# Kernel tuning notes

Measured on AMD Instinct MI355X. Metric: run time of the kernel, lower is better.

The kernel has to match this reference:

```python
import jax, jax.numpy as jnp
import numpy as np

NUM_EXPERTS = 8
EMBED_DIM = 512
NUM_LAYERS = 2
LN_EPS = 1e-5


def _all_pairs_hyperedges(E):
    # static 'all_pairs' strategy: one hyperedge per unordered expert pair
    nodes, edges = [], []
    eid = 0
    for i in range(E):
        for j in range(i + 1, E):
            nodes += [i, j]
            edges += [eid, eid]
            eid += 1
    return np.asarray(nodes, np.int32), np.asarray(edges, np.int32)


def setup_inputs() -> dict:
    key = jax.random.key(0)
    ks = jax.random.split(key, 4)
    B, L, E, D = 8, 1024, NUM_EXPERTS, EMBED_DIM
    nodes, edges = _all_pairs_hyperedges(E)
    return {
        "expert_outputs": jax.random.normal(ks[0], (B, L, E, D), jnp.float32),
        # HypergraphConv: lin has bias=False, conv bias is separate
        "hgnn_w": jax.random.normal(ks[1], (NUM_LAYERS, D, D), jnp.float32) * 0.02,
        "hgnn_b": jnp.zeros((NUM_LAYERS, D), jnp.float32),
        # combiner: Linear(D,D) -> GELU -> LayerNorm(D)
        "comb_w": jax.random.normal(ks[2], (D, D), jnp.float32) * 0.02,
        "comb_b": jnp.zeros((D,), jnp.float32),
        "ln_gamma": jnp.ones((D,), jnp.float32),
        "ln_beta": jnp.zeros((D,), jnp.float32),
        "nodes_idx": jnp.asarray(nodes),
        "edges_idx": jnp.asarray(edges),
    }


def _hypergraph_conv(h, W, b, nodes_idx, edges_idx, num_edges, d_inv, b_inv):
    # h: [N, E, D] with N = B*L token-graphs sharing the static hyperedge structure.
    # PyG HypergraphConv (no attention, unit edge weights):
    #   out = D^{-1} H B^{-1} H^T (h @ W^T) + b
    x = jnp.einsum('ned,fd->nef', h, W)  # lin(x), bias=False
    N, E, D = x.shape
    # node -> hyperedge scatter-add, scaled by inverse hyperedge degree B^{-1}
    m = jnp.zeros((N, num_edges, D), x.dtype)
    m = m.at[:, edges_idx].add(x[:, nodes_idx]) * b_inv[None, :, None]
    # hyperedge -> node scatter-add, scaled by inverse node degree D^{-1}
    out = jnp.zeros((N, E, D), x.dtype)
    out = out.at[:, nodes_idx].add(m[:, edges_idx]) * d_inv[None, :, None]
    return out + b


def reference(expert_outputs, hgnn_w, hgnn_b, comb_w, comb_b, ln_gamma, ln_beta, nodes_idx, edges_idx):
    B, L, E, D = expert_outputs.shape
    num_edges = nodes_idx.shape[0] // 2  # all_pairs: exactly 2 nodes per hyperedge
    # degree normalizations (unit hyperedge weights)
    deg = jnp.zeros((E,), expert_outputs.dtype).at[nodes_idx].add(1.0)
    d_inv = jnp.where(deg > 0, 1.0 / deg, 0.0)
    edeg = jnp.zeros((num_edges,), expert_outputs.dtype).at[edges_idx].add(1.0)
    b_inv = jnp.where(edeg > 0, 1.0 / edeg, 0.0)

    h = expert_outputs.reshape(B * L, E, D)
    for l in range(hgnn_w.shape[0]):
        h = _hypergraph_conv(h, hgnn_w[l], hgnn_b[l], nodes_idx, edges_idx, num_edges, d_inv, b_inv)

    pooled = h.reshape(B, L, E, D).mean(axis=2)  # [B, L, D]
    z = jax.nn.gelu(pooled @ comb_w.T + comb_b, approximate=False)  # torch nn.GELU = exact
    mu = jnp.mean(z, axis=-1, keepdims=True)
    var = jnp.var(z, axis=-1, keepdims=True)
    return (z - mu) / jnp.sqrt(var + LN_EPS) * ln_gamma + ln_beta
```

## Files before the change

kernel.cpp:

```cpp
#include <hip/hip_runtime.h>
#include <hip/hip_bf16.h>
#include <math.h>


#define DD 512
#define NTOK 8192

typedef short s16x8 __attribute__((ext_vector_type(8)));
typedef short s16x4 __attribute__((ext_vector_type(4)));
typedef float f32x4 __attribute__((ext_vector_type(4)));

static __device__ __forceinline__ short f2bf(float x) {
  unsigned u = __builtin_bit_cast(unsigned, x);
  unsigned r = (u + 0x7fffu + ((u >> 16) & 1u)) >> 16;
  return (short)r;
}

static __device__ __forceinline__ void do_cast4(const float* __restrict__ src,
                                                short* __restrict__ dst, int i) {
  int j = i << 2;
  f32x4 v = *(const f32x4*)(src + j);
  s16x4 o;
  o[0] = f2bf(v[0]); o[1] = f2bf(v[1]); o[2] = f2bf(v[2]); o[3] = f2bf(v[3]);
  *(s16x4*)(dst + j) = o;
}

static __device__ __forceinline__ void do_mv(const float* __restrict__ M,
                                             const float* __restrict__ v,
                                             const float* __restrict__ add,
                                             float* __restrict__ outv,
                                             int gtid) {
  int w = gtid >> 6, l = gtid & 63;
  if (w >= DD) return;
  float s = 0.f;
  for (int k = l; k < DD; k += 64) s += M[(size_t)w * DD + k] * v[k];
#pragma unroll
  for (int m = 32; m; m >>= 1) s += __shfl_xor(s, m);
  if (l == 0) outv[w] = s + add[w];
}

__global__ __launch_bounds__(256) void prep1_kernel(
    const float* __restrict__ w1, const float* __restrict__ w2,
    const float* __restrict__ wc, const float* __restrict__ b1,
    const float* __restrict__ b2, short* __restrict__ w1t,
    short* __restrict__ w2b, short* __restrict__ wcb,
    float* __restrict__ tmpv) {
  int b = blockIdx.x, tid = threadIdx.x;
  if (b < 256) {
    __shared__ float t[32][33];
    int bx = b & 15, by = b >> 4;
    int tx = tid & 31, ty8 = tid >> 5;
    int r0 = by * 32, c0 = bx * 32;
#pragma unroll
    for (int j = 0; j < 4; ++j) {
      int r = ty8 * 4 + j;
      t[r][tx] = w1[(size_t)(r0 + r) * DD + c0 + tx];
    }
    __syncthreads();
#pragma unroll
    for (int j = 0; j < 4; ++j) {
      int r = ty8 * 4 + j;
      w1t[(size_t)(c0 + r) * DD + r0 + tx] = f2bf(t[tx][r]);
    }
  } else if (b < 768) {
    int i = (b - 256) * 256 + tid;
    if (i < 65536) do_cast4(w2, w2b, i);
    else           do_cast4(wc, wcb, i - 65536);
  } else {
    do_mv(w2, b1, b2, tmpv, (b - 768) * 256 + tid);
  }
}

static __device__ __forceinline__ void do_wgemm(const short* __restrict__ A,
                                                const short* __restrict__ B,
                                                short* __restrict__ Out,
                                                int b, int tid) {
  int w = tid >> 6, l = tid & 63;
  int lr = l & 15, lg = l >> 4;
  int m0 = (b >> 3) * 64 + w * 16;
  int n0 = (b & 7) * 64;
  f32x4 acc[4] = {};
  const short* ap = A + (size_t)(m0 + lr) * DD + 8 * lg;
  const short* bp = B + (size_t)(n0 + lr) * DD + 8 * lg;
#pragma unroll
  for (int k0 = 0; k0 < DD; k0 += 32) {
    s16x8 a = *(const s16x8*)(ap + k0);
#pragma unroll
    for (int f = 0; f < 4; ++f) {
      s16x8 bb = *(const s16x8*)(bp + (size_t)f * 16 * DD + k0);
      acc[f] = __builtin_amdgcn_mfma_f32_16x16x32_bf16(a, bb, acc[f], 0, 0, 0);
    }
  }
#pragma unroll
  for (int f = 0; f < 4; ++f)
#pragma unroll
    for (int r = 0; r < 4; ++r)
      Out[(size_t)(m0 + lg * 4 + r) * DD + n0 + f * 16 + lr] = f2bf(acc[f][r]);
}

__global__ __launch_bounds__(256) void prep2_kernel(
    const short* __restrict__ w1t, const short* __restrict__ w2b,
    short* __restrict__ w21t, const float* __restrict__ wc,
    const float* __restrict__ tmpv, const float* __restrict__ cb,
    float* __restrict__ cbias) {
  int b = blockIdx.x, tid = threadIdx.x;
  if (b < 64) do_wgemm(w1t, w2b, w21t, b, tid);
  else        do_mv(wc, tmpv, cb, cbias, (b - 64) * 256 + tid);
}

__global__ __launch_bounds__(256) void prep3_kernel(const short* __restrict__ wcb,
                                                    const short* __restrict__ w21t,
                                                    short* __restrict__ wcomb) {
  do_wgemm(wcb, w21t, wcomb, blockIdx.x, threadIdx.x);
}

__global__ __launch_bounds__(512, 8) void main_kernel(
    const float* __restrict__ x, const short* __restrict__ wcomb,
    const float* __restrict__ cbias, const float* __restrict__ gamma,
    const float* __restrict__ beta, float* __restrict__ out) {
  __shared__ short As[8 * DD];
  __shared__ float red[8][8][2];
  int tid = threadIdx.x;
  int w = tid >> 6, l = tid & 63;
  int lr = l & 15, lg = l >> 4;
  int m0 = blockIdx.x * 8;

  {
    const float* xb = x + (size_t)m0 * (8 * DD);
    char* ls = (char*)As;
#pragma unroll
    for (int j = 0; j < 2; ++j) {
      int i = tid + 512 * j;
      int n = i >> 7;
      int d4 = (i & 127) << 2;
      const float* p = xb + n * (8 * DD) + d4;
      f32x4 s = {0.f, 0.f, 0.f, 0.f};
#pragma unroll
      for (int e = 0; e < 8; ++e) s += *(const f32x4*)(p + e * DD);
      s *= 0.125f;
      s16x4 o;
      o[0] = f2bf(s[0]); o[1] = f2bf(s[1]); o[2] = f2bf(s[2]); o[3] = f2bf(s[3]);
      int bo = d4 << 1;
      *(s16x4*)(ls + n * 1024 + (bo ^ ((n & 7) << 4))) = o;
    }
  }
  __syncthreads();

  f32x4 acc[4] = {};
  int arow = lr & 7;
  const short* bbase = wcomb + (size_t)(w * 64 + lr) * DD + 8 * lg;
  const char* lsc = (const char*)As;
  for (int k0 = 0; k0 < DD; k0 += 32) {
    int kb = (k0 + 8 * lg) * 2;
    s16x8 a = *(const s16x8*)(lsc + arow * 1024 + (kb ^ (arow << 4)));
#pragma unroll
    for (int f = 0; f < 4; ++f) {
      s16x8 b = *(const s16x8*)(bbase + (size_t)f * 16 * DD + k0);
      acc[f] = __builtin_amdgcn_mfma_f32_16x16x32_bf16(a, b, acc[f], 0, 0, 0);
    }
  }

  int cbase = w * 64 + lr;
  float s1[4] = {}, s2[4] = {};
#pragma unroll
  for (int f = 0; f < 4; ++f) {
    float cb = cbias[cbase + f * 16];
#pragma unroll
    for (int r = 0; r < 4; ++r) {
      float xx = acc[f][r] + cb;
      float z = 0.5f * xx * (1.0f + erff(xx * 0.70710678118f));
      acc[f][r] = z;
      s1[r] += z;
      s2[r] += z * z;
    }
  }
#pragma unroll
  for (int m = 1; m < 16; m <<= 1)
#pragma unroll
    for (int r = 0; r < 4; ++r) {
      s1[r] += __shfl_xor(s1[r], m);
      s2[r] += __shfl_xor(s2[r], m);
    }
  if (lr == 0 && lg < 2) {
#pragma unroll
    for (int r = 0; r < 4; ++r) {
      int row = lg * 4 + r;
      red[row][w][0] = s1[r];
      red[row][w][1] = s2[r];
    }
  }
  __syncthreads();
  if (lg < 2) {
#pragma unroll
    for (int r = 0; r < 4; ++r) {
      int row = lg * 4 + r;
      float t1 = 0.f, t2 = 0.f;
#pragma unroll
      for (int ww = 0; ww < 8; ++ww) {
        t1 += red[row][ww][0];
        t2 += red[row][ww][1];
      }
      float mu = t1 * (1.0f / 512.0f);
      float var = t2 * (1.0f / 512.0f) - mu * mu;
      float rs = rsqrtf(var + 1e-5f);
      float* op = out + (size_t)(m0 + row) * DD;
#pragma unroll
      for (int f = 0; f < 4; ++f) {
        int c = cbase + f * 16;
        op[c] = (acc[f][r] - mu) * rs * gamma[c] + beta[c];
      }
    }
  }
}

extern "C" void kernel_launch(void* const* d_in, const int* in_sizes, int n_in,
                              void* d_out, int out_size, void* d_ws, size_t ws_size,
                              hipStream_t stream) {
  const float* x   = (const float*)d_in[0];
  const float* hw  = (const float*)d_in[1];
  const float* hb  = (const float*)d_in[2];
  const float* cw  = (const float*)d_in[3];
  const float* cb  = (const float*)d_in[4];
  const float* gam = (const float*)d_in[5];
  const float* bet = (const float*)d_in[6];
  float* out = (float*)d_out;

  char* ws = (char*)d_ws;
  short* w1t   = (short*)ws; ws += DD * DD * 2;
  short* w2b   = (short*)ws; ws += DD * DD * 2;
  short* wcb   = (short*)ws; ws += DD * DD * 2;
  short* w21t  = (short*)ws; ws += DD * DD * 2;
  short* wcomb = (short*)ws; ws += DD * DD * 2;
  float* tmpv  = (float*)ws; ws += DD * 4;
  float* cbias = (float*)ws; ws += DD * 4;

  const float* W1 = hw;
  const float* W2 = hw + DD * DD;
  const float* b1 = hb;
  const float* b2 = hb + DD;

  prep1_kernel<<<896, 256, 0, stream>>>(W1, W2, cw, b1, b2, w1t, w2b, wcb, tmpv);
  prep2_kernel<<<192, 256, 0, stream>>>(w1t, w2b, w21t, cw, tmpv, cb, cbias);
  prep3_kernel<<<64, 256, 0, stream>>>(wcb, w21t, wcomb);
  main_kernel<<<NTOK / 8, 512, 0, stream>>>(x, wcomb, cbias, gam, bet, out);
}
```

Baseline: 282.7 us.

## Move expert mean-pooling into prep kernel and use 16-row GEMM tiles

The expert-axis mean and bf16 cast now run as extra blocks of the first prep kernel and write a pooled bf16 buffer to workspace. That streaming read of the 128 MB input overlaps with the weight preprocessing instead of waiting behind the prep3 chain. The GEMM+LayerNorm kernel then loads pre-pooled rows and processes 16 tokens per block, filling all 16 MFMA rows instead of duplicating 8. The cost is an extra global write and read of the pooled activations and lower occupancy hints.

```diff
diff --git a/kernel.cpp b/kernel.cpp
--- a/kernel.cpp
+++ b/kernel.cpp
@@ -42,11 +42,27 @@
 __global__ __launch_bounds__(256) void prep1_kernel(
     const float* __restrict__ w1, const float* __restrict__ w2,
     const float* __restrict__ wc, const float* __restrict__ b1,
-    const float* __restrict__ b2, short* __restrict__ w1t,
-    short* __restrict__ w2b, short* __restrict__ wcb,
-    float* __restrict__ tmpv) {
+    const float* __restrict__ b2, const float* __restrict__ x,
+    short* __restrict__ w1t, short* __restrict__ w2b, short* __restrict__ wcb,
+    float* __restrict__ tmpv, short* __restrict__ g) {
   int b = blockIdx.x, tid = threadIdx.x;
-  if (b < 256) {
+  if (b >= 896) {
+    int i0 = (b - 896) * 256 + tid;
+#pragma unroll
+    for (int j = 0; j < 2; ++j) {
+      int ci = i0 + j * 524288;
+      int n = ci >> 7;
+      int d4 = (ci & 127) << 2;
+      const float* p = x + (size_t)n * (8 * DD) + d4;
+      f32x4 s = {0.f, 0.f, 0.f, 0.f};
+#pragma unroll
+      for (int e = 0; e < 8; ++e) s += *(const f32x4*)(p + e * DD);
+      s *= 0.125f;
+      s16x4 o;
+      o[0] = f2bf(s[0]); o[1] = f2bf(s[1]); o[2] = f2bf(s[2]); o[3] = f2bf(s[3]);
+      *(s16x4*)(g + (size_t)n * DD + d4) = o;
+    }
+  } else if (b < 256) {
     __shared__ float t[32][33];
     int bx = b & 15, by = b >> 4;
     int tx = tid & 31, ty8 = tid >> 5;
@@ -114,45 +130,37 @@
   do_wgemm(wcb, w21t, wcomb, blockIdx.x, threadIdx.x);
 }
 
-__global__ __launch_bounds__(512, 8) void main_kernel(
-    const float* __restrict__ x, const short* __restrict__ wcomb,
+__global__ __launch_bounds__(512, 4) void gemm_ln_kernel(
+    const short* __restrict__ g, const short* __restrict__ wcomb,
     const float* __restrict__ cbias, const float* __restrict__ gamma,
     const float* __restrict__ beta, float* __restrict__ out) {
-  __shared__ short As[8 * DD];
-  __shared__ float red[8][8][2];
+  __shared__ short As[16 * DD];
+  __shared__ float red[16][8][2];
   int tid = threadIdx.x;
   int w = tid >> 6, l = tid & 63;
   int lr = l & 15, lg = l >> 4;
-  int m0 = blockIdx.x * 8;
+  int m0 = blockIdx.x * 16;
 
   {
-    const float* xb = x + (size_t)m0 * (8 * DD);
+    const char* gs = (const char*)(g + (size_t)m0 * DD);
     char* ls = (char*)As;
 #pragma unroll
     for (int j = 0; j < 2; ++j) {
-      int i = tid + 512 * j;
-      int n = i >> 7;
-      int d4 = (i & 127) << 2;
-      const float* p = xb + n * (8 * DD) + d4;
-      f32x4 s = {0.f, 0.f, 0.f, 0.f};
-#pragma unroll
-      for (int e = 0; e < 8; ++e) s += *(const f32x4*)(p + e * DD);
-      s *= 0.125f;
-      s16x4 o;
-      o[0] = f2bf(s[0]); o[1] = f2bf(s[1]); o[2] = f2bf(s[2]); o[3] = f2bf(s[3]);
-      int bo = d4 << 1;
-      *(s16x4*)(ls + n * 1024 + (bo ^ ((n & 7) << 4))) = o;
+      int ci = tid + 512 * j;
+      int row = ci >> 6;
+      int bo = (ci & 63) << 4;
+      s16x8 v = *(const s16x8*)(gs + row * 1024 + bo);
+      *(s16x8*)(ls + row * 1024 + (bo ^ ((row & 7) << 4))) = v;
     }
   }
   __syncthreads();
 
   f32x4 acc[4] = {};
-  int arow = lr & 7;
   const short* bbase = wcomb + (size_t)(w * 64 + lr) * DD + 8 * lg;
   const char* lsc = (const char*)As;
   for (int k0 = 0; k0 < DD; k0 += 32) {
     int kb = (k0 + 8 * lg) * 2;
-    s16x8 a = *(const s16x8*)(lsc + arow * 1024 + (kb ^ (arow << 4)));
+    s16x8 a = *(const s16x8*)(lsc + lr * 1024 + (kb ^ ((lr & 7) << 4)));
 #pragma unroll
     for (int f = 0; f < 4; ++f) {
       s16x8 b = *(const s16x8*)(bbase + (size_t)f * 16 * DD + k0);
@@ -181,7 +189,7 @@
       s1[r] += __shfl_xor(s1[r], m);
       s2[r] += __shfl_xor(s2[r], m);
     }
-  if (lr == 0 && lg < 2) {
+  if (lr == 0) {
 #pragma unroll
     for (int r = 0; r < 4; ++r) {
       int row = lg * 4 + r;
@@ -190,25 +198,23 @@
     }
   }
   __syncthreads();
-  if (lg < 2) {
-#pragma unroll
-    for (int r = 0; r < 4; ++r) {
-      int row = lg * 4 + r;
-      float t1 = 0.f, t2 = 0.f;
-#pragma unroll
-      for (int ww = 0; ww < 8; ++ww) {
-        t1 += red[row][ww][0];
-        t2 += red[row][ww][1];
-      }
-      float mu = t1 * (1.0f / 512.0f);
-      float var = t2 * (1.0f / 512.0f) - mu * mu;
-      float rs = rsqrtf(var + 1e-5f);
-      float* op = out + (size_t)(m0 + row) * DD;
-#pragma unroll
-      for (int f = 0; f < 4; ++f) {
-        int c = cbase + f * 16;
-        op[c] = (acc[f][r] - mu) * rs * gamma[c] + beta[c];
-      }
+#pragma unroll
+  for (int r = 0; r < 4; ++r) {
+    int row = lg * 4 + r;
+    float t1 = 0.f, t2 = 0.f;
+#pragma unroll
+    for (int ww = 0; ww < 8; ++ww) {
+      t1 += red[row][ww][0];
+      t2 += red[row][ww][1];
+    }
+    float mu = t1 * (1.0f / 512.0f);
+    float var = t2 * (1.0f / 512.0f) - mu * mu;
+    float rs = rsqrtf(var + 1e-5f);
+    float* op = out + (size_t)(m0 + row) * DD;
+#pragma unroll
+    for (int f = 0; f < 4; ++f) {
+      int c = cbase + f * 16;
+      op[c] = (acc[f][r] - mu) * rs * gamma[c] + beta[c];
     }
   }
 }
@@ -226,6 +232,7 @@
   float* out = (float*)d_out;
 
   char* ws = (char*)d_ws;
+  short* g     = (short*)ws; ws += (size_t)NTOK * DD * 2;
   short* w1t   = (short*)ws; ws += DD * DD * 2;
   short* w2b   = (short*)ws; ws += DD * DD * 2;
   short* wcb   = (short*)ws; ws += DD * DD * 2;
@@ -239,8 +246,9 @@
   const float* b1 = hb;
   const float* b2 = hb + DD;
 
-  prep1_kernel<<<896, 256, 0, stream>>>(W1, W2, cw, b1, b2, w1t, w2b, wcb, tmpv);
+  prep1_kernel<<<2944, 256, 0, stream>>>(W1, W2, cw, b1, b2, x,
+                                         w1t, w2b, wcb, tmpv, g);
   prep2_kernel<<<192, 256, 0, stream>>>(w1t, w2b, w21t, cw, tmpv, cb, cbias);
   prep3_kernel<<<64, 256, 0, stream>>>(wcb, w21t, wcomb);
-  main_kernel<<<NTOK / 8, 512, 0, stream>>>(x, wcomb, cbias, gam, bet, out);
-}
+  gemm_ln_kernel<<<NTOK / 16, 512, 0, stream>>>(g, wcomb, cbias, gam, bet, out);
+}
```

Result: faster. 265.1 us (-6.2%).
